# Performance work log

Measured on AMD Instinct MI355X. Metric: run time of the kernel, lower is better.

## Reference

```python
import jax, jax.numpy as jnp
import numpy as np
from jax import lax

B, IN, H1, H2, NC = 16384, 128, 256, 128, 10
BETA = 0.5
THR = 1.0
SLOPE = 25.0  # snntorch surrogate.fast_sigmoid default slope


@jax.custom_vjp
def spike(x):
    # Heaviside fire with fast-sigmoid surrogate gradient
    return (x > 0).astype(x.dtype)

def _spike_fwd(x):
    return spike(x), x

def _spike_bwd(x, g):
    return (g / (SLOPE * jnp.abs(x) + 1.0) ** 2,)

spike.defvjp(_spike_fwd, _spike_bwd)


def setup_inputs() -> dict:
    key = jax.random.key(0)
    ks = jax.random.split(key, 7)
    def lin(kw, kb, fan_in, fan_out):
        lim = 1.0 / np.sqrt(fan_in)
        W = jax.random.uniform(kw, (fan_out, fan_in), jnp.float32, -lim, lim)
        b = jax.random.uniform(kb, (fan_out,), jnp.float32, -lim, lim)
        return W, b
    W1, b1 = lin(ks[0], ks[1], IN, H1)
    W2, b2 = lin(ks[2], ks[3], H1, H2)
    Wo, bo = lin(ks[4], ks[5], H2, NC)
    x = jax.random.normal(ks[6], (B, IN), jnp.float32)
    return {"x": x, "W1": W1, "b1": b1, "W2": W2, "b2": b2,
            "Wo": Wo, "bo": bo, "num_steps": 20}


def reference(x, W1, b1, W2, b2, Wo, bo, num_steps):
    # fc1(x) is time-invariant -> hoist out of the recurrent loop (same math)
    cur1 = x @ W1.T + b1  # [B, H1]

    def lif(mem, cur):
        # snntorch Leaky (reset_mechanism='subtract'):
        # reset from previous mem (detached), then decay+input, then fire
        reset = lax.stop_gradient((mem > THR).astype(mem.dtype))
        mem = BETA * mem + cur - reset * THR
        spk = spike(mem - THR)
        return spk, mem

    def step(carry, _):
        m1, m2, mo = carry
        s1, m1 = lif(m1, cur1)
        s2, m2 = lif(m2, s1 @ W2.T + b2)
        so, mo = lif(mo, s2 @ Wo.T + bo)
        return (m1, m2, mo), so

    init = (jnp.zeros((B, H1), x.dtype),
            jnp.zeros((B, H2), x.dtype),
            jnp.zeros((B, NC), x.dtype))
    _, spk_rec = lax.scan(step, init, None, length=num_steps)
    return spk_rec.sum(axis=0)  # [B, NC] spike counts
```

## Files before the change

kernel.cpp:

```cpp
#include <hip/hip_runtime.h>
#include <stdint.h>

#define B_TOT 16384
#define IN_DIM 128
#define H1 256
#define H2 128
#define NC 10

#define W2T_BYTES (257 * H2 * 4)
#define WOT_OFF   W2T_BYTES
#define SCR_OFF   136768
#define LDS_BYTES (SCR_OFF + 16 * 1024)

#define JDUMMY 256
#define ODUMMY 128

typedef float v2f __attribute__((ext_vector_type(2)));

__global__ __launch_bounds__(256) void gemm1_kernel(
    const float* __restrict__ x, const float* __restrict__ W1,
    const float* __restrict__ b1, float* __restrict__ cur1) {
  __shared__ float xs[16 * 128];
  const int tid = threadIdx.x;
  const long row0 = (long)blockIdx.x * 16;

  const float4* xt = (const float4*)(x + row0 * IN_DIM);
  float4* xs4 = (float4*)xs;
  xs4[tid] = xt[tid];
  xs4[tid + 256] = xt[tid + 256];
  __syncthreads();

  const int n = tid;
  float acc[16];
#pragma unroll
  for (int r = 0; r < 16; ++r) acc[r] = 0.f;

  const float* wrow = W1 + n * IN_DIM;
  for (int k0 = 0; k0 < IN_DIM; k0 += 4) {
    const float4 wv = *(const float4*)(wrow + k0);
#pragma unroll
    for (int r = 0; r < 16; ++r) {
      const float4 xv = *(const float4*)(xs + r * IN_DIM + k0);
      acc[r] = fmaf(wv.x, xv.x, acc[r]);
      acc[r] = fmaf(wv.y, xv.y, acc[r]);
      acc[r] = fmaf(wv.z, xv.z, acc[r]);
      acc[r] = fmaf(wv.w, xv.w, acc[r]);
    }
  }
  const float bias = b1[n];
#pragma unroll
  for (int r = 0; r < 16; ++r)
    cur1[(row0 + r) * H1 + n] = acc[r] + bias;
}

__global__ __launch_bounds__(1024) void transpose_kernel(
    const float* __restrict__ W2, const float* __restrict__ Wo,
    float* __restrict__ W2T, float* __restrict__ WoT) {
  const int idx = blockIdx.x * 1024 + threadIdx.x;
  if (idx < H2 * H1) {
    const int o = idx >> 8;
    const int j = idx & 255;
    W2T[j * H2 + o] = W2[idx];
  } else {
    const int k = idx - H2 * H1;
    if (k < NC * H2) {
      const int o = k >> 7;
      const int j = k & 127;
      WoT[j * NC + o] = Wo[k];
    }
  }
}

__device__ __forceinline__ int mbcnt64(unsigned long long m) {
  return (int)__builtin_amdgcn_mbcnt_hi(
      (unsigned)(m >> 32), __builtin_amdgcn_mbcnt_lo((unsigned)m, 0u));
}

__global__ __launch_bounds__(1024) void snn_kernel(
    const float* __restrict__ cur1, const float* __restrict__ W2Tg,
    const float* __restrict__ WoTg, const float* __restrict__ b2,
    const float* __restrict__ bo, const int* __restrict__ nsp,
    float* __restrict__ out) {
  extern __shared__ float lds[];

  const int tid = threadIdx.x;
  {
    float4* dst = (float4*)lds;
    const float4* src = (const float4*)W2Tg;
#pragma unroll
    for (int i = 0; i < 8; ++i) dst[tid + i * 1024] = src[tid + i * 1024];
    if (tid < 320)
      ((float4*)((char*)lds + WOT_OFF))[tid] = ((const float4*)WoTg)[tid];
    if (tid < 32)
      ((float4*)((char*)lds))[256 * 32 + tid] = make_float4(0.f, 0.f, 0.f, 0.f);
    if (tid < NC) ((float*)((char*)lds + WOT_OFF))[128 * NC + tid] = 0.f;
  }
  __syncthreads();

  const int w = tid >> 6;
  const int l = tid & 63;
  const int lo = (l < NC) ? l : 0;
  const float bb0 = b2[2 * l];
  const float bb1 = b2[2 * l + 1];
  const float bol = bo[lo];
  const int nsteps = *nsp;

  unsigned short* scrA = (unsigned short*)((char*)lds + SCR_OFF) + w * 512;
  unsigned short* scrB = scrA + 256;
  const char* w2p = (const char*)lds + 8 * l;
  const char* wop = (const char*)lds + WOT_OFF + 4 * lo;

#define LOAD8(P, scrp, kidx)                                              \
  const int4 P##i = *(const int4*)((const char*)(scrp) + (kidx) * 16);    \
  const int P##j0 = P##i.x & 0xffff;                                      \
  const int P##j1 = ((unsigned)P##i.x) >> 16;                             \
  const int P##j2 = P##i.y & 0xffff;                                      \
  const int P##j3 = ((unsigned)P##i.y) >> 16;                             \
  const int P##j4 = P##i.z & 0xffff;                                      \
  const int P##j5 = ((unsigned)P##i.z) >> 16;                             \
  const int P##j6 = P##i.w & 0xffff;                                      \
  const int P##j7 = ((unsigned)P##i.w) >> 16;                             \
  const v2f P##p0 = *(const v2f*)(w2p + (P##j0 << 9));                    \
  const v2f P##p1 = *(const v2f*)(w2p + (P##j1 << 9));                    \
  const v2f P##p2 = *(const v2f*)(w2p + (P##j2 << 9));                    \
  const v2f P##p3 = *(const v2f*)(w2p + (P##j3 << 9));                    \
  const v2f P##p4 = *(const v2f*)(w2p + (P##j4 << 9));                    \
  const v2f P##p5 = *(const v2f*)(w2p + (P##j5 << 9));                    \
  const v2f P##p6 = *(const v2f*)(w2p + (P##j6 << 9));                    \
  const v2f P##p7 = *(const v2f*)(w2p + (P##j7 << 9));

#define ADD8(P, acc)                                                      \
  acc += P##p0; acc += P##p1; acc += P##p2; acc += P##p3;                 \
  acc += P##p4; acc += P##p5; acc += P##p6; acc += P##p7;

#define OLOAD8(P, scrp, kidx)                                             \
  const int4 P##i = *(const int4*)((const char*)(scrp) + (kidx) * 16);    \
  const int P##j0 = P##i.x & 0xffff;                                      \
  const int P##j1 = ((unsigned)P##i.x) >> 16;                             \
  const int P##j2 = P##i.y & 0xffff;                                      \
  const int P##j3 = ((unsigned)P##i.y) >> 16;                             \
  const int P##j4 = P##i.z & 0xffff;                                      \
  const int P##j5 = ((unsigned)P##i.z) >> 16;                             \
  const int P##j6 = P##i.w & 0xffff;                                      \
  const int P##j7 = ((unsigned)P##i.w) >> 16;                             \
  const float P##q0 = *(const float*)(wop + P##j0 * 40);                  \
  const float P##q1 = *(const float*)(wop + P##j1 * 40);                  \
  const float P##q2 = *(const float*)(wop + P##j2 * 40);                  \
  const float P##q3 = *(const float*)(wop + P##j3 * 40);                  \
  const float P##q4 = *(const float*)(wop + P##j4 * 40);                  \
  const float P##q5 = *(const float*)(wop + P##j5 * 40);                  \
  const float P##q6 = *(const float*)(wop + P##j6 * 40);                  \
  const float P##q7 = *(const float*)(wop + P##j7 * 40);

#define OADD8(P, co)                                                      \
  co += P##q0; co += P##q1; co += P##q2; co += P##q3;                     \
  co += P##q4; co += P##q5; co += P##q6; co += P##q7;

  for (int rp = 0; rp < 2; ++rp) {
    const long bA = (long)blockIdx.x * 64 + w * 4 + rp * 2;
    const long bB = bA + 1;

    float cA[4], cB[4];
#pragma unroll
    for (int i = 0; i < 4; ++i) {
      cA[i] = cur1[bA * H1 + i * 64 + l];
      cB[i] = cur1[bB * H1 + i * 64 + l];
    }

    float mA1[4] = {0.f, 0.f, 0.f, 0.f}, spA1[4] = {0.f, 0.f, 0.f, 0.f};
    float mB1[4] = {0.f, 0.f, 0.f, 0.f}, spB1[4] = {0.f, 0.f, 0.f, 0.f};
    float mA2a = 0.f, mA2b = 0.f, spA2a = 0.f, spA2b = 0.f;
    float mB2a = 0.f, mB2b = 0.f, spB2a = 0.f, spB2b = 0.f;
    float moA = 0.f, spoA = 0.f, cntA = 0.f;
    float moB = 0.f, spoB = 0.f, cntB = 0.f;

    for (int t = 0; t < nsteps; ++t) {
      unsigned long long gA[4], gB[4];
      bool sA[4], sB[4];
#pragma unroll
      for (int i = 0; i < 4; ++i) {
        mA1[i] = fmaf(0.5f, mA1[i], cA[i]) - spA1[i];
        sA[i] = mA1[i] > 1.0f;
        spA1[i] = sA[i] ? 1.0f : 0.0f;
        gA[i] = __ballot(sA[i]);
        mB1[i] = fmaf(0.5f, mB1[i], cB[i]) - spB1[i];
        sB[i] = mB1[i] > 1.0f;
        spB1[i] = sB[i] ? 1.0f : 0.0f;
        gB[i] = __ballot(sB[i]);
      }
      const int pA0 = (int)__popcll(gA[0]);
      const int pA01 = pA0 + (int)__popcll(gA[1]);
      const int pA012 = pA01 + (int)__popcll(gA[2]);
      const int SA = pA012 + (int)__popcll(gA[3]);
      const int pB0 = (int)__popcll(gB[0]);
      const int pB01 = pB0 + (int)__popcll(gB[1]);
      const int pB012 = pB01 + (int)__popcll(gB[2]);
      const int SB = pB012 + (int)__popcll(gB[3]);

      if (sA[0]) scrA[mbcnt64(gA[0])] = (unsigned short)l;
      if (sA[1]) scrA[pA0 + mbcnt64(gA[1])] = (unsigned short)(64 + l);
      if (sA[2]) scrA[pA01 + mbcnt64(gA[2])] = (unsigned short)(128 + l);
      if (sA[3]) scrA[pA012 + mbcnt64(gA[3])] = (unsigned short)(192 + l);
      if (sB[0]) scrB[mbcnt64(gB[0])] = (unsigned short)l;
      if (sB[1]) scrB[pB0 + mbcnt64(gB[1])] = (unsigned short)(64 + l);
      if (sB[2]) scrB[pB01 + mbcnt64(gB[2])] = (unsigned short)(128 + l);
      if (sB[3]) scrB[pB012 + mbcnt64(gB[3])] = (unsigned short)(192 + l);
      const int padA = (8 - (SA & 7)) & 7;
      const int padB = (8 - (SB & 7)) & 7;
      if (l < padA) scrA[SA + l] = JDUMMY;
      if (l < padB) scrB[SB + l] = JDUMMY;
      asm volatile("s_waitcnt lgkmcnt(0)" ::: "memory");

      v2f accA = {0.f, 0.f}, accB = {0.f, 0.f};
      {
        const int nA = (SA + 7) >> 3;
        const int nB = (SB + 7) >> 3;
        int ka = 0, kb = 0;
        while (ka < nA && kb < nB) {
          LOAD8(a_, scrA, ka)
          LOAD8(b_, scrB, kb)
          ADD8(a_, accA)
          ADD8(b_, accB)
          ++ka;
          ++kb;
        }
        while (ka < nA) {
          LOAD8(c_, scrA, ka)
          ADD8(c_, accA)
          ++ka;
        }
        while (kb < nB) {
          LOAD8(d_, scrB, kb)
          ADD8(d_, accB)
          ++kb;
        }
      }
      const float aA0 = accA.x + bb0;
      const float aA1 = accA.y + bb1;
      const float aB0 = accB.x + bb0;
      const float aB1 = accB.y + bb1;

      mA2a = fmaf(0.5f, mA2a, aA0) - spA2a;
      mA2b = fmaf(0.5f, mA2b, aA1) - spA2b;
      mB2a = fmaf(0.5f, mB2a, aB0) - spB2a;
      mB2b = fmaf(0.5f, mB2b, aB1) - spB2b;
      const bool saA = mA2a > 1.0f, sbA = mA2b > 1.0f;
      const bool saB = mB2a > 1.0f, sbB = mB2b > 1.0f;
      const unsigned long long mAe = __ballot(saA);
      const unsigned long long mAo = __ballot(sbA);
      const unsigned long long mBe = __ballot(saB);
      const unsigned long long mBo = __ballot(sbB);
      spA2a = saA ? 1.0f : 0.0f;
      spA2b = sbA ? 1.0f : 0.0f;
      spB2a = saB ? 1.0f : 0.0f;
      spB2b = sbB ? 1.0f : 0.0f;
      const int pAe = (int)__popcll(mAe);
      const int SoA = pAe + (int)__popcll(mAo);
      const int pBe = (int)__popcll(mBe);
      const int SoB = pBe + (int)__popcll(mBo);

      if (saA) scrA[mbcnt64(mAe)] = (unsigned short)(2 * l);
      if (sbA) scrA[pAe + mbcnt64(mAo)] = (unsigned short)(2 * l + 1);
      if (saB) scrB[mbcnt64(mBe)] = (unsigned short)(2 * l);
      if (sbB) scrB[pBe + mbcnt64(mBo)] = (unsigned short)(2 * l + 1);
      const int padOA = (8 - (SoA & 7)) & 7;
      const int padOB = (8 - (SoB & 7)) & 7;
      if (l < padOA) scrA[SoA + l] = ODUMMY;
      if (l < padOB) scrB[SoB + l] = ODUMMY;
      asm volatile("s_waitcnt lgkmcnt(0)" ::: "memory");

      float coA = 0.f, coB = 0.f;
      {
        const int nA = (SoA + 7) >> 3;
        const int nB = (SoB + 7) >> 3;
        int ka = 0, kb = 0;
        while (ka < nA && kb < nB) {
          OLOAD8(e_, scrA, ka)
          OLOAD8(f_, scrB, kb)
          OADD8(e_, coA)
          OADD8(f_, coB)
          ++ka;
          ++kb;
        }
        while (ka < nA) {
          OLOAD8(g_, scrA, ka)
          OADD8(g_, coA)
          ++ka;
        }
        while (kb < nB) {
          OLOAD8(h_, scrB, kb)
          OADD8(h_, coB)
          ++kb;
        }
      }
      coA += bol;
      coB += bol;

      moA = fmaf(0.5f, moA, coA) - spoA;
      moB = fmaf(0.5f, moB, coB) - spoB;
      const bool soA = moA > 1.0f;
      const bool soB = moB > 1.0f;
      spoA = soA ? 1.0f : 0.0f;
      spoB = soB ? 1.0f : 0.0f;
      cntA += spoA;
      cntB += spoB;
    }

    if (l < NC) {
      out[bA * NC + l] = cntA;
      out[bB * NC + l] = cntB;
    }
  }
#undef LOAD8
#undef ADD8
#undef OLOAD8
#undef OADD8
}

extern "C" void kernel_launch(void* const* d_in, const int* in_sizes, int n_in,
                              void* d_out, int out_size, void* d_ws,
                              size_t ws_size, hipStream_t stream) {
  const float* x  = (const float*)d_in[0];
  const float* W1 = (const float*)d_in[1];
  const float* b1 = (const float*)d_in[2];
  const float* W2 = (const float*)d_in[3];
  const float* b2 = (const float*)d_in[4];
  const float* Wo = (const float*)d_in[5];
  const float* bo = (const float*)d_in[6];
  const int* nsp  = (const int*)d_in[7];
  float* outp = (float*)d_out;

  float* cur1 = (float*)d_ws;
  float* W2Tg = cur1 + (size_t)B_TOT * H1;
  float* WoTg = W2Tg + H1 * H2;

  gemm1_kernel<<<B_TOT / 16, 256, 0, stream>>>(x, W1, b1, cur1);
  transpose_kernel<<<(H2 * H1 + NC * H2 + 1023) / 1024, 1024, 0, stream>>>(
      W2, Wo, W2Tg, WoTg);

  hipFuncSetAttribute((const void*)snn_kernel,
                      hipFuncAttributeMaxDynamicSharedMemorySize, LDS_BYTES);
  snn_kernel<<<256, 1024, LDS_BYTES, stream>>>(cur1, W2Tg, WoTg, b2, bo, nsp,
                                               outp);
}
```

Measured before the change: 137.5 us.

## Store precomputed byte offsets in spike index lists and drop dummy padding

The compacted spike lists now hold 32-bit precomputed LDS byte offsets instead of 16-bit neuron indices, so the gather loops skip the unpack, shift and multiply on each entry. The dummy zero rows and pad writes are removed, and leftover entries are handled by 4/2/1 tail blocks. Because 32-bit entries need twice the scratch space, a list capped at 128 entries falls back to a noinline bitmask-walk routine when more than 128 layer-1 neurons fire, which adds branching and divergence risk.

```diff
diff --git a/kernel.cpp b/kernel.cpp
--- a/kernel.cpp
+++ b/kernel.cpp
@@ -7,13 +7,11 @@
 #define H2 128
 #define NC 10
 
-#define W2T_BYTES (257 * H2 * 4)
+#define W2T_BYTES (H1 * H2 * 4)
 #define WOT_OFF   W2T_BYTES
-#define SCR_OFF   136768
+#define WOT_BYTES (H2 * NC * 4)
+#define SCR_OFF   (WOT_OFF + WOT_BYTES)
 #define LDS_BYTES (SCR_OFF + 16 * 1024)
-
-#define JDUMMY 256
-#define ODUMMY 128
 
 typedef float v2f __attribute__((ext_vector_type(2)));
 
@@ -76,6 +74,23 @@
       (unsigned)(m >> 32), __builtin_amdgcn_mbcnt_lo((unsigned)m, 0u));
 }
 
+__device__ __noinline__ v2f serial_row(unsigned long long m0,
+                                       unsigned long long m1,
+                                       unsigned long long m2,
+                                       unsigned long long m3,
+                                       const char* w2b) {
+  v2f acc = {0.f, 0.f};
+  while (m0) { const int j = (int)__builtin_ctzll(m0); m0 &= m0 - 1;
+    acc += *(const v2f*)(w2b + (j << 9)); }
+  while (m1) { const int j = (int)__builtin_ctzll(m1); m1 &= m1 - 1;
+    acc += *(const v2f*)(w2b + ((64 + j) << 9)); }
+  while (m2) { const int j = (int)__builtin_ctzll(m2); m2 &= m2 - 1;
+    acc += *(const v2f*)(w2b + ((128 + j) << 9)); }
+  while (m3) { const int j = (int)__builtin_ctzll(m3); m3 &= m3 - 1;
+    acc += *(const v2f*)(w2b + ((192 + j) << 9)); }
+  return acc;
+}
+
 __global__ __launch_bounds__(1024) void snn_kernel(
     const float* __restrict__ cur1, const float* __restrict__ W2Tg,
     const float* __restrict__ WoTg, const float* __restrict__ b2,
@@ -91,9 +106,6 @@
     for (int i = 0; i < 8; ++i) dst[tid + i * 1024] = src[tid + i * 1024];
     if (tid < 320)
       ((float4*)((char*)lds + WOT_OFF))[tid] = ((const float4*)WoTg)[tid];
-    if (tid < 32)
-      ((float4*)((char*)lds))[256 * 32 + tid] = make_float4(0.f, 0.f, 0.f, 0.f);
-    if (tid < NC) ((float*)((char*)lds + WOT_OFF))[128 * NC + tid] = 0.f;
   }
   __syncthreads();
 
@@ -105,56 +117,98 @@
   const float bol = bo[lo];
   const int nsteps = *nsp;
 
-  unsigned short* scrA = (unsigned short*)((char*)lds + SCR_OFF) + w * 512;
-  unsigned short* scrB = scrA + 256;
-  const char* w2p = (const char*)lds + 8 * l;
-  const char* wop = (const char*)lds + WOT_OFF + 4 * lo;
-
-#define LOAD8(P, scrp, kidx)                                              \
-  const int4 P##i = *(const int4*)((const char*)(scrp) + (kidx) * 16);    \
-  const int P##j0 = P##i.x & 0xffff;                                      \
-  const int P##j1 = ((unsigned)P##i.x) >> 16;                             \
-  const int P##j2 = P##i.y & 0xffff;                                      \
-  const int P##j3 = ((unsigned)P##i.y) >> 16;                             \
-  const int P##j4 = P##i.z & 0xffff;                                      \
-  const int P##j5 = ((unsigned)P##i.z) >> 16;                             \
-  const int P##j6 = P##i.w & 0xffff;                                      \
-  const int P##j7 = ((unsigned)P##i.w) >> 16;                             \
-  const v2f P##p0 = *(const v2f*)(w2p + (P##j0 << 9));                    \
-  const v2f P##p1 = *(const v2f*)(w2p + (P##j1 << 9));                    \
-  const v2f P##p2 = *(const v2f*)(w2p + (P##j2 << 9));                    \
-  const v2f P##p3 = *(const v2f*)(w2p + (P##j3 << 9));                    \
-  const v2f P##p4 = *(const v2f*)(w2p + (P##j4 << 9));                    \
-  const v2f P##p5 = *(const v2f*)(w2p + (P##j5 << 9));                    \
-  const v2f P##p6 = *(const v2f*)(w2p + (P##j6 << 9));                    \
-  const v2f P##p7 = *(const v2f*)(w2p + (P##j7 << 9));
-
-#define ADD8(P, acc)                                                      \
-  acc += P##p0; acc += P##p1; acc += P##p2; acc += P##p3;                 \
+  int* scrA = (int*)((char*)lds + SCR_OFF) + w * 256;
+  int* scrB = scrA + 128;
+  const char* w2b = (const char*)lds + 8 * l;
+  const char* wob = (const char*)lds + WOT_OFF + 4 * lo;
+
+  const int wr0 = l << 9;
+  const int wr1 = (64 + l) << 9;
+  const int wr2 = (128 + l) << 9;
+  const int wr3 = (192 + l) << 9;
+  const int or0 = 80 * l;
+  const int or1 = 80 * l + 40;
+
+#define LOAD8(P, scrp, kk)                                  \
+  const int4 P##ia = *(const int4*)((scrp) + (kk));         \
+  const int4 P##ib = *(const int4*)((scrp) + (kk) + 4);     \
+  const v2f P##p0 = *(const v2f*)(w2b + P##ia.x);           \
+  const v2f P##p1 = *(const v2f*)(w2b + P##ia.y);           \
+  const v2f P##p2 = *(const v2f*)(w2b + P##ia.z);           \
+  const v2f P##p3 = *(const v2f*)(w2b + P##ia.w);           \
+  const v2f P##p4 = *(const v2f*)(w2b + P##ib.x);           \
+  const v2f P##p5 = *(const v2f*)(w2b + P##ib.y);           \
+  const v2f P##p6 = *(const v2f*)(w2b + P##ib.z);           \
+  const v2f P##p7 = *(const v2f*)(w2b + P##ib.w);
+
+#define ADD8(P, acc)                                        \
+  acc += P##p0; acc += P##p1; acc += P##p2; acc += P##p3;   \
   acc += P##p4; acc += P##p5; acc += P##p6; acc += P##p7;
 
-#define OLOAD8(P, scrp, kidx)                                             \
-  const int4 P##i = *(const int4*)((const char*)(scrp) + (kidx) * 16);    \
-  const int P##j0 = P##i.x & 0xffff;                                      \
-  const int P##j1 = ((unsigned)P##i.x) >> 16;                             \
-  const int P##j2 = P##i.y & 0xffff;                                      \
-  const int P##j3 = ((unsigned)P##i.y) >> 16;                             \
-  const int P##j4 = P##i.z & 0xffff;                                      \
-  const int P##j5 = ((unsigned)P##i.z) >> 16;                             \
-  const int P##j6 = P##i.w & 0xffff;                                      \
-  const int P##j7 = ((unsigned)P##i.w) >> 16;                             \
-  const float P##q0 = *(const float*)(wop + P##j0 * 40);                  \
-  const float P##q1 = *(const float*)(wop + P##j1 * 40);                  \
-  const float P##q2 = *(const float*)(wop + P##j2 * 40);                  \
-  const float P##q3 = *(const float*)(wop + P##j3 * 40);                  \
-  const float P##q4 = *(const float*)(wop + P##j4 * 40);                  \
-  const float P##q5 = *(const float*)(wop + P##j5 * 40);                  \
-  const float P##q6 = *(const float*)(wop + P##j6 * 40);                  \
-  const float P##q7 = *(const float*)(wop + P##j7 * 40);
-
-#define OADD8(P, co)                                                      \
-  co += P##q0; co += P##q1; co += P##q2; co += P##q3;                     \
+#define TAILS(scrp, S, acc)                                 \
+  {                                                         \
+    int k = ((S) >> 3) << 3;                                \
+    if ((S) & 4) {                                          \
+      const int4 ia = *(const int4*)((scrp) + k);           \
+      const v2f p0 = *(const v2f*)(w2b + ia.x);             \
+      const v2f p1 = *(const v2f*)(w2b + ia.y);             \
+      const v2f p2 = *(const v2f*)(w2b + ia.z);             \
+      const v2f p3 = *(const v2f*)(w2b + ia.w);             \
+      acc += p0; acc += p1; acc += p2; acc += p3;           \
+      k += 4;                                               \
+    }                                                       \
+    if ((S) & 2) {                                          \
+      const int2 ia = *(const int2*)((scrp) + k);           \
+      const v2f p0 = *(const v2f*)(w2b + ia.x);             \
+      const v2f p1 = *(const v2f*)(w2b + ia.y);             \
+      acc += p0; acc += p1;                                 \
+      k += 2;                                               \
+    }                                                       \
+    if ((S) & 1) {                                          \
+      const v2f p0 = *(const v2f*)(w2b + (scrp)[k]);        \
+      acc += p0;                                            \
+    }                                                       \
+  }
+
+#define OLOAD8(P, scrp, kk)                                 \
+  const int4 P##ia = *(const int4*)((scrp) + (kk));         \
+  const int4 P##ib = *(const int4*)((scrp) + (kk) + 4);     \
+  const float P##q0 = *(const float*)(wob + P##ia.x);       \
+  const float P##q1 = *(const float*)(wob + P##ia.y);       \
+  const float P##q2 = *(const float*)(wob + P##ia.z);       \
+  const float P##q3 = *(const float*)(wob + P##ia.w);       \
+  const float P##q4 = *(const float*)(wob + P##ib.x);       \
+  const float P##q5 = *(const float*)(wob + P##ib.y);       \
+  const float P##q6 = *(const float*)(wob + P##ib.z);       \
+  const float P##q7 = *(const float*)(wob + P##ib.w);
+
+#define OADD8(P, co)                                        \
+  co += P##q0; co += P##q1; co += P##q2; co += P##q3;       \
   co += P##q4; co += P##q5; co += P##q6; co += P##q7;
+
+#define OTAILS(scrp, S, co)                                 \
+  {                                                         \
+    int k = ((S) >> 3) << 3;                                \
+    if ((S) & 4) {                                          \
+      const int4 ia = *(const int4*)((scrp) + k);           \
+      const float u0 = *(const float*)(wob + ia.x);         \
+      const float u1 = *(const float*)(wob + ia.y);         \
+      const float u2 = *(const float*)(wob + ia.z);         \
+      const float u3 = *(const float*)(wob + ia.w);         \
+      co += u0; co += u1; co += u2; co += u3;               \
+      k += 4;                                               \
+    }                                                       \
+    if ((S) & 2) {                                          \
+      const int2 ia = *(const int2*)((scrp) + k);           \
+      const float u0 = *(const float*)(wob + ia.x);         \
+      const float u1 = *(const float*)(wob + ia.y);         \
+      co += u0; co += u1;                                   \
+      k += 2;                                               \
+    }                                                       \
+    if ((S) & 1) {                                          \
+      co += *(const float*)(wob + (scrp)[k]);               \
+    }                                                       \
+  }
 
   for (int rp = 0; rp < 2; ++rp) {
     const long bA = (long)blockIdx.x * 64 + w * 4 + rp * 2;
@@ -197,43 +251,43 @@
       const int pB012 = pB01 + (int)__popcll(gB[2]);
       const int SB = pB012 + (int)__popcll(gB[3]);
 
-      if (sA[0]) scrA[mbcnt64(gA[0])] = (unsigned short)l;
-      if (sA[1]) scrA[pA0 + mbcnt64(gA[1])] = (unsigned short)(64 + l);
-      if (sA[2]) scrA[pA01 + mbcnt64(gA[2])] = (unsigned short)(128 + l);
-      if (sA[3]) scrA[pA012 + mbcnt64(gA[3])] = (unsigned short)(192 + l);
-      if (sB[0]) scrB[mbcnt64(gB[0])] = (unsigned short)l;
-      if (sB[1]) scrB[pB0 + mbcnt64(gB[1])] = (unsigned short)(64 + l);
-      if (sB[2]) scrB[pB01 + mbcnt64(gB[2])] = (unsigned short)(128 + l);
-      if (sB[3]) scrB[pB012 + mbcnt64(gB[3])] = (unsigned short)(192 + l);
-      const int padA = (8 - (SA & 7)) & 7;
-      const int padB = (8 - (SB & 7)) & 7;
-      if (l < padA) scrA[SA + l] = JDUMMY;
-      if (l < padB) scrB[SB + l] = JDUMMY;
+      if (sA[0]) scrA[mbcnt64(gA[0])] = wr0;
+      if (sA[1]) scrA[pA0 + mbcnt64(gA[1])] = wr1;
+      if (sA[2]) { const int rk = pA01 + mbcnt64(gA[2]);
+                   if (rk < 128) scrA[rk] = wr2; }
+      if (sA[3]) { const int rk = pA012 + mbcnt64(gA[3]);
+                   if (rk < 128) scrA[rk] = wr3; }
+      if (sB[0]) scrB[mbcnt64(gB[0])] = wr0;
+      if (sB[1]) scrB[pB0 + mbcnt64(gB[1])] = wr1;
+      if (sB[2]) { const int rk = pB01 + mbcnt64(gB[2]);
+                   if (rk < 128) scrB[rk] = wr2; }
+      if (sB[3]) { const int rk = pB012 + mbcnt64(gB[3]);
+                   if (rk < 128) scrB[rk] = wr3; }
       asm volatile("s_waitcnt lgkmcnt(0)" ::: "memory");
 
       v2f accA = {0.f, 0.f}, accB = {0.f, 0.f};
-      {
-        const int nA = (SA + 7) >> 3;
-        const int nB = (SB + 7) >> 3;
+      if (__builtin_expect(SA > 128 || SB > 128, 0)) {
+        accA = serial_row(gA[0], gA[1], gA[2], gA[3], w2b);
+        accB = serial_row(gB[0], gB[1], gB[2], gB[3], w2b);
+      } else {
+        const int nA8 = SA >> 3;
+        const int nB8 = SB >> 3;
         int ka = 0, kb = 0;
-        while (ka < nA && kb < nB) {
-          LOAD8(a_, scrA, ka)
-          LOAD8(b_, scrB, kb)
-          ADD8(a_, accA)
-          ADD8(b_, accB)
+        while (ka < nA8 && kb < nB8) {
+          { LOAD8(a_, scrA, ka * 8) LOAD8(b_, scrB, kb * 8)
+            ADD8(a_, accA) ADD8(b_, accB) }
+          ++ka; ++kb;
+        }
+        while (ka < nA8) {
+          { LOAD8(c_, scrA, ka * 8) ADD8(c_, accA) }
           ++ka;
+        }
+        while (kb < nB8) {
+          { LOAD8(d_, scrB, kb * 8) ADD8(d_, accB) }
           ++kb;
         }
-        while (ka < nA) {
-          LOAD8(c_, scrA, ka)
-          ADD8(c_, accA)
-          ++ka;
-        }
-        while (kb < nB) {
-          LOAD8(d_, scrB, kb)
-          ADD8(d_, accB)
-          ++kb;
-        }
+        TAILS(scrA, SA, accA)
+        TAILS(scrB, SB, accB)
       }
       const float aA0 = accA.x + bb0;
       const float aA1 = accA.y + bb1;
@@ -259,39 +313,32 @@
       const int pBe = (int)__popcll(mBe);
       const int SoB = pBe + (int)__popcll(mBo);
 
-      if (saA) scrA[mbcnt64(mAe)] = (unsigned short)(2 * l);
-      if (sbA) scrA[pAe + mbcnt64(mAo)] = (unsigned short)(2 * l + 1);
-      if (saB) scrB[mbcnt64(mBe)] = (unsigned short)(2 * l);
-      if (sbB) scrB[pBe + mbcnt64(mBo)] = (unsigned short)(2 * l + 1);
-      const int padOA = (8 - (SoA & 7)) & 7;
-      const int padOB = (8 - (SoB & 7)) & 7;
-      if (l < padOA) scrA[SoA + l] = ODUMMY;
-      if (l < padOB) scrB[SoB + l] = ODUMMY;
+      if (saA) scrA[mbcnt64(mAe)] = or0;
+      if (sbA) scrA[pAe + mbcnt64(mAo)] = or1;
+      if (saB) scrB[mbcnt64(mBe)] = or0;
+      if (sbB) scrB[pBe + mbcnt64(mBo)] = or1;
       asm volatile("s_waitcnt lgkmcnt(0)" ::: "memory");
 
       float coA = 0.f, coB = 0.f;
       {
-        const int nA = (SoA + 7) >> 3;
-        const int nB = (SoB + 7) >> 3;
+        const int nA8 = SoA >> 3;
+        const int nB8 = SoB >> 3;
         int ka = 0, kb = 0;
-        while (ka < nA && kb < nB) {
-          OLOAD8(e_, scrA, ka)
-          OLOAD8(f_, scrB, kb)
-          OADD8(e_, coA)
-          OADD8(f_, coB)
+        while (ka < nA8 && kb < nB8) {
+          { OLOAD8(e_, scrA, ka * 8) OLOAD8(f_, scrB, kb * 8)
+            OADD8(e_, coA) OADD8(f_, coB) }
+          ++ka; ++kb;
+        }
+        while (ka < nA8) {
+          { OLOAD8(g_, scrA, ka * 8) OADD8(g_, coA) }
           ++ka;
+        }
+        while (kb < nB8) {
+          { OLOAD8(h_, scrB, kb * 8) OADD8(h_, coB) }
           ++kb;
         }
-        while (ka < nA) {
-          OLOAD8(g_, scrA, ka)
-          OADD8(g_, coA)
-          ++ka;
-        }
-        while (kb < nB) {
-          OLOAD8(h_, scrB, kb)
-          OADD8(h_, coB)
-          ++kb;
-        }
+        OTAILS(scrA, SoA, coA)
+        OTAILS(scrB, SoB, coB)
       }
       coA += bol;
       coB += bol;
@@ -313,8 +360,10 @@
   }
 #undef LOAD8
 #undef ADD8
+#undef TAILS
 #undef OLOAD8
 #undef OADD8
+#undef OTAILS
 }
 
 extern "C" void kernel_launch(void* const* d_in, const int* in_sizes, int n_in,
```

After: 115.4 us (median of 3 runs). 16.0% less time.
